# Optimization experiments

Measured on AMD Instinct MI355X. Metric: run time of the kernel, lower is better.

Reference implementation:

```python
import jax, jax.numpy as jnp
import numpy as np
jax.config.update("jax_enable_x64", True)

B, N, FEAT_DIM, OUT_DIM = 16, 10000, 256, 256
CH = [3, 64, 64, 64, 128, FEAT_DIM]  # ptlk PointNet_features MLP widths (scale=1)
BN_EPS = 1e-5
L2_EPS = 1e-12


def setup_inputs() -> dict:
    key = jax.random.key(0)
    ks = jax.random.split(key, 2 * len(CH) + 4)
    inp = {"points": jax.random.normal(ks[0], (B, N, 3), dtype=jnp.float32)}
    for i in range(5):
        cin, cout = CH[i], CH[i + 1]
        inp[f"W{i}"] = jax.random.normal(ks[1 + 2 * i], (cout, cin), dtype=jnp.float32) / np.sqrt(cin).astype(np.float32)
        inp[f"g{i}"] = jnp.ones((cout,), jnp.float32)
        inp[f"b{i}"] = jnp.zeros((cout,), jnp.float32)
    inp["Wfc"] = jax.random.normal(ks[-2], (OUT_DIM, FEAT_DIM * FEAT_DIM), dtype=jnp.float32) / np.sqrt(FEAT_DIM * FEAT_DIM).astype(np.float32)
    inp["bfc"] = jnp.zeros((OUT_DIM,), jnp.float32)
    return inp


def _bn_relu(y, g, b):
    # training-mode BatchNorm1d over (batch, points) per channel; y: [B,C,N]
    mu = jnp.mean(y, axis=(0, 2), keepdims=True)
    var = jnp.var(y, axis=(0, 2), keepdims=True)
    y = (y - mu) * jax.lax.rsqrt(var + BN_EPS)
    return jax.nn.relu(y * g[None, :, None] + b[None, :, None])


def reference(points, W0, g0, b0, W1, g1, b1, W2, g2, b2, W3, g3, b3, W4, g4, b4, Wfc, bfc):
    x = jnp.transpose(points, (0, 2, 1))  # [B,3,N]
    for W, g, b in ((W0, g0, b0), (W1, g1, b1), (W2, g2, b2), (W3, g3, b3), (W4, g4, b4)):
        x = jnp.einsum('oc,bcn->bon', W, x)  # 1x1 conv1d
        x = _bn_relu(x, g, b)
    f = jnp.transpose(x, (0, 2, 1))  # [B,N,D] per-point features
    # so_cov: global mean over all B*N points (as in the original), then per-batch covariance
    mean = jnp.mean(f.reshape(-1, FEAT_DIM), axis=0)  # [D]
    fc = f - mean
    cov = jnp.einsum('bnd,bne->bde', fc, fc) / np.float32(N)  # [B,D,D]
    # matrix square-root via fp64 SVD (torch: x.double(); u s v = svd; u diag(s^0.5) v^T)
    u, s, vh = jnp.linalg.svd(cov.astype(jnp.float64), full_matrices=False)
    sqrt_cov = (u * jnp.sqrt(s)[:, None, :]) @ vh  # [B,D,D]
    v = sqrt_cov.reshape(f.shape[0], FEAT_DIM * FEAT_DIM).astype(jnp.float32)
    out = v @ Wfc.T + bfc  # [B,OUT_DIM]
    norm = jnp.maximum(jnp.linalg.norm(out, axis=-1, keepdims=True), L2_EPS)
    return out / norm
```

## Files before the change

### kernel.cpp

```cpp
#include <hip/hip_runtime.h>
#include <cmath>

constexpr int NB   = 16;
constexpr int NPTS = 10000;
constexpr int NBN  = NB * NPTS;
constexpr int NS_ITERS = 18;
constexpr int COV_CHUNKS = 20;
constexpr int CHUNK_PTS  = 500;
constexpr int COV_KK     = 16;

typedef _Float16 f16x8 __attribute__((ext_vector_type(8)));
typedef float  f32x4  __attribute__((ext_vector_type(4)));
typedef unsigned short ushort4v __attribute__((ext_vector_type(4)));
typedef unsigned short ushort8v __attribute__((ext_vector_type(8)));

__global__ __launch_bounds__(256) void conv0_ker(const float* __restrict__ pts,
                                                 const float* __restrict__ W,
                                                 float* __restrict__ y) {
    int g = blockIdx.x * 256 + threadIdx.x;
    int b = g / NPTS;
    int n = g - b * NPTS;
    float p0 = pts[3 * (size_t)g + 0];
    float p1 = pts[3 * (size_t)g + 1];
    float p2 = pts[3 * (size_t)g + 2];
    float* yp = y + ((size_t)b * 64) * NPTS + n;
    for (int o = 0; o < 64; ++o) {
        float v = W[3 * o] * p0 + W[3 * o + 1] * p1 + W[3 * o + 2] * p2;
        yp[(size_t)o * NPTS] = v;
    }
}

__device__ __forceinline__ unsigned short f2h(float f) {
    return __builtin_bit_cast(unsigned short, (_Float16)f);
}
__device__ __forceinline__ float hres(float f) {
    return f - (float)(_Float16)f;
}
__device__ __forceinline__ int swzu(int us) {
    return us ^ (((us >> 7) & 3) << 4);
}

template <int CIN, int COUT, int OTILE>
__global__ __launch_bounds__(256) void conv_mfma(const float* __restrict__ xin,
                                                 const float* __restrict__ ss,
                                                 const float* __restrict__ W,
                                                 float* __restrict__ y) {
    constexpr int OT = OTILE / 16;
    constexpr int WM = 4;
    constexpr int WN = (OTILE == 128) ? 4 : 2;
    __shared__ unsigned short Xp[2][8 * 512];
    __shared__ unsigned short Wp[2][OT * 512];

    const int tid  = threadIdx.x;
    const int lane = tid & 63;
    const int w    = tid >> 6;
    const int wr   = (OTILE == 128) ? (w & 1) : 0;
    const int wc   = (OTILE == 128) ? (w >> 1) : w;

    const int nb = blockIdx.x * 128;
    const int ob = blockIdx.y * OTILE;
    const int b  = blockIdx.z;

    f32x4 acc[WM][WN];
#pragma unroll
    for (int m = 0; m < WM; ++m)
#pragma unroll
        for (int n = 0; n < WN; ++n) acc[m][n] = (f32x4){0.f, 0.f, 0.f, 0.f};

    const int xn = tid & 127;
    const int th = tid >> 7;
    const bool nok = (nb + xn) < NPTS;

#pragma unroll 1
    for (int kc = 0; kc < CIN; kc += 32) {
        __syncthreads();
#pragma unroll
        for (int i = 0; i < OTILE / 32; ++i) {
            int l = i * 256 + tid;
            int o = l >> 3, k4 = (l & 7) << 2;
            float4 v = *(const float4*)(W + (size_t)(ob + o) * CIN + kc + k4);
            ushort4v h4, l4;
            h4[0] = f2h(v.x); l4[0] = f2h(hres(v.x));
            h4[1] = f2h(v.y); l4[1] = f2h(hres(v.y));
            h4[2] = f2h(v.z); l4[2] = f2h(hres(v.z));
            h4[3] = f2h(v.w); l4[3] = f2h(hres(v.w));
            int us = swzu((o >> 4) * 512 + ((k4 >> 3) * 16 + (o & 15)) * 8 + (k4 & 7));
            *(ushort4v*)&Wp[0][us] = h4;
            *(ushort4v*)&Wp[1][us] = l4;
        }
#pragma unroll
        for (int qq = 0; qq < 2; ++qq) {
            int q = th * 2 + qq;
            const float* xb = xin + ((size_t)(b * CIN + kc + q * 8)) * NPTS + nb + xn;
            float f[8];
#pragma unroll
            for (int j = 0; j < 8; ++j) {
                float v = nok ? xb[(size_t)j * NPTS] : 0.f;
                int c = kc + q * 8 + j;
                f[j] = fmaxf(fmaf(v, ss[c], ss[256 + c]), 0.f);
            }
            ushort8v h8, l8;
#pragma unroll
            for (int j = 0; j < 8; ++j) {
                h8[j] = f2h(f[j]);
                l8[j] = f2h(hres(f[j]));
            }
            int us = swzu((xn >> 4) * 512 + (q * 16 + (xn & 15)) * 8);
            *(ushort8v*)&Xp[0][us] = h8;
            *(ushort8v*)&Xp[1][us] = l8;
        }
        __syncthreads();

        f16x8 ah[WM], al[WM], bh[WN], bl[WN];
#pragma unroll
        for (int m = 0; m < WM; ++m) {
            int us = swzu((wr * WM + m) * 512 + lane * 8);
            ah[m] = *(const f16x8*)&Wp[0][us];
            al[m] = *(const f16x8*)&Wp[1][us];
        }
#pragma unroll
        for (int n = 0; n < WN; ++n) {
            int us = swzu((wc * WN + n) * 512 + lane * 8);
            bh[n] = *(const f16x8*)&Xp[0][us];
            bl[n] = *(const f16x8*)&Xp[1][us];
        }
#pragma unroll
        for (int m = 0; m < WM; ++m)
#pragma unroll
            for (int n = 0; n < WN; ++n) {
                acc[m][n] = __builtin_amdgcn_mfma_f32_16x16x32_f16(ah[m], bh[n], acc[m][n], 0, 0, 0);
                acc[m][n] = __builtin_amdgcn_mfma_f32_16x16x32_f16(ah[m], bl[n], acc[m][n], 0, 0, 0);
                acc[m][n] = __builtin_amdgcn_mfma_f32_16x16x32_f16(al[m], bh[n], acc[m][n], 0, 0, 0);
            }
    }

    const int ro = (lane >> 4) * 4;
    const int co = lane & 15;
#pragma unroll
    for (int m = 0; m < WM; ++m) {
        int o = ob + wr * (WM * 16) + m * 16 + ro;
#pragma unroll
        for (int n = 0; n < WN; ++n) {
            int col = nb + wc * (WN * 16) + n * 16 + co;
            if (col < NPTS) {
                float* yp = y + ((size_t)(b * COUT + o)) * NPTS + col;
#pragma unroll
                for (int r = 0; r < 4; ++r)
                    yp[(size_t)r * NPTS] = acc[m][n][r];
            }
        }
    }
}

__global__ void chan_stats(const float* __restrict__ y, int C, float* __restrict__ stats) {
    int c = blockIdx.x, b = blockIdx.y, t = threadIdx.x;
    const float* p = y + ((size_t)(b * C + c)) * NPTS;
    float s = 0.f, q = 0.f;
    for (int n = t; n < NPTS; n += 256) {
        float v = p[n];
        s += v;
        q = fmaf(v, v, q);
    }
    for (int off = 32; off; off >>= 1) {
        s += __shfl_down(s, off);
        q += __shfl_down(q, off);
    }
    __shared__ float ls[4], lq[4];
    if ((t & 63) == 0) { ls[t >> 6] = s; lq[t >> 6] = q; }
    __syncthreads();
    if (t == 0) {
        atomicAdd(&stats[c],     ls[0] + ls[1] + ls[2] + ls[3]);
        atomicAdd(&stats[C + c], lq[0] + lq[1] + lq[2] + lq[3]);
    }
}

__global__ void bn_finalize(const float* __restrict__ stats, const float* __restrict__ g,
                            const float* __restrict__ bi, int C, float* __restrict__ ss) {
    int c = threadIdx.x;
    if (c < C) {
        float mu  = stats[c] * (1.f / NBN);
        float var = stats[C + c] * (1.f / NBN) - mu * mu;
        float r = rsqrtf(var + 1e-5f);
        float s = g[c] * r;
        ss[c] = s;
        ss[256 + c] = bi[c] - mu * s;
    }
}

__device__ __forceinline__ int swz8(int byteoff) {
    return byteoff ^ (((byteoff >> 8) & 3) << 5);
}

__global__ __launch_bounds__(256) void cov_mfma(const float* __restrict__ y4,
                                                const float* __restrict__ ss,
                                                float* __restrict__ covP,
                                                float* __restrict__ fsumb) {
    __shared__ unsigned short pan[2][2][4096];

    const int chunk = blockIdx.x;
    const int tile  = blockIdx.y;
    const int b     = blockIdx.z;
    const int ti = (tile == 1) ? 1 : 0;
    const int tj = (tile == 0) ? 0 : 1;
    const int npan = (tile == 2) ? 2 : 1;

    const int tid  = threadIdx.x;
    const int lane = tid & 63;
    const int w    = tid >> 6;
    const int wr   = w & 1, wc = w >> 1;

    const int n0c = chunk * CHUNK_PTS;

    f32x4 acc[4][4];
#pragma unroll
    for (int m = 0; m < 4; ++m)
#pragma unroll
        for (int n = 0; n < 4; ++n) acc[m][n] = (f32x4){0.f, 0.f, 0.f, 0.f};

    const int g   = tid & 7;
    const int chb = tid >> 3;
    const int p4  = g * 4;
    const int q   = p4 >> 3, j0 = p4 & 7;

    float fs[4] = {0.f, 0.f, 0.f, 0.f};

#pragma unroll 1
    for (int kk = 0; kk < COV_KK; ++kk) {
        const int nbase = n0c + kk * 32;
        __syncthreads();
        for (int p = 0; p < npan; ++p) {
            const int pcb = (p ? tj : ti) * 128;
#pragma unroll
            for (int i = 0; i < 4; ++i) {
                const int ch = chb + 32 * i;
                float4 v = make_float4(0.f, 0.f, 0.f, 0.f);
                if (kk * 32 + p4 < CHUNK_PTS) {
                    v = *(const float4*)(y4 + ((size_t)(b * 256 + pcb + ch)) * NPTS + nbase + p4);
                    float sc = ss[pcb + ch], sh = ss[256 + pcb + ch];
                    v.x = fmaxf(fmaf(v.x, sc, sh), 0.f);
                    v.y = fmaxf(fmaf(v.y, sc, sh), 0.f);
                    v.z = fmaxf(fmaf(v.z, sc, sh), 0.f);
                    v.w = fmaxf(fmaf(v.w, sc, sh), 0.f);
                }
                if (npan == 1) fs[i] += (v.x + v.y) + (v.z + v.w);
                ushort4v h4, l4;
                h4[0] = f2h(v.x); l4[0] = f2h(hres(v.x));
                h4[1] = f2h(v.y); l4[1] = f2h(hres(v.y));
                h4[2] = f2h(v.z); l4[2] = f2h(hres(v.z));
                h4[3] = f2h(v.w); l4[3] = f2h(hres(v.w));
                const int addr = (ch >> 4) * 512 + (q * 16 + (ch & 15)) * 8 + j0;
                const int sa = swz8(addr * 2) >> 1;
                *(ushort4v*)&pan[p][0][sa] = h4;
                *(ushort4v*)&pan[p][1][sa] = l4;
            }
        }
        __syncthreads();

        const unsigned short* Ah = pan[0][0];
        const unsigned short* Al = pan[0][1];
        const unsigned short* Bh = pan[npan - 1][0];
        const unsigned short* Bl = pan[npan - 1][1];

        f16x8 ah[4], al[4], bh[4], bl[4];
#pragma unroll
        for (int m = 0; m < 4; ++m) {
            int t8 = (wr * 4 + m) * 512 + lane * 8;
            int sa = swz8(t8 * 2) >> 1;
            ah[m] = *(const f16x8*)&Ah[sa];
            al[m] = *(const f16x8*)&Al[sa];
        }
#pragma unroll
        for (int n = 0; n < 4; ++n) {
            int t8 = (wc * 4 + n) * 512 + lane * 8;
            int sa = swz8(t8 * 2) >> 1;
            bh[n] = *(const f16x8*)&Bh[sa];
            bl[n] = *(const f16x8*)&Bl[sa];
        }
#pragma unroll
        for (int m = 0; m < 4; ++m)
#pragma unroll
            for (int n = 0; n < 4; ++n) {
                acc[m][n] = __builtin_amdgcn_mfma_f32_16x16x32_f16(ah[m], bh[n], acc[m][n], 0, 0, 0);
                acc[m][n] = __builtin_amdgcn_mfma_f32_16x16x32_f16(ah[m], bl[n], acc[m][n], 0, 0, 0);
                acc[m][n] = __builtin_amdgcn_mfma_f32_16x16x32_f16(al[m], bh[n], acc[m][n], 0, 0, 0);
            }
    }

    if (npan == 1) {
#pragma unroll
        for (int i = 0; i < 4; ++i) {
            float s = fs[i];
            s += __shfl_xor(s, 1);
            s += __shfl_xor(s, 2);
            s += __shfl_xor(s, 4);
            if (g == 0)
                atomicAdd(&fsumb[b * 256 + ti * 128 + chb + 32 * i], s);
        }
    }

    float* outp = covP + (((size_t)(chunk * NB + b) * 3 + tile) << 14);
    const int rowb = wr * 64;
    const int colb = wc * 64;
#pragma unroll
    for (int m = 0; m < 4; ++m)
#pragma unroll
        for (int n = 0; n < 4; ++n)
#pragma unroll
            for (int r = 0; r < 4; ++r) {
                int row = rowb + m * 16 + (lane >> 4) * 4 + r;
                int col = colb + n * 16 + (lane & 15);
                outp[(row << 7) + col] = acc[m][n][r];
            }
}

__global__ void covfin_ker(const float* __restrict__ covP, const float* __restrict__ fsumb,
                           float* __restrict__ Y0, float* __restrict__ trace) {
    int r = blockIdx.x, b = blockIdx.y, c = threadIdx.x;
    float fbr = fsumb[b * 256 + r] * (1.f / NPTS);
    float fbc = fsumb[b * 256 + c] * (1.f / NPTS);
    float mr = 0.f, mc = 0.f;
    for (int q = 0; q < NB; ++q) {
        mr += fsumb[q * 256 + r];
        mc += fsumb[q * 256 + c];
    }
    mr *= (1.f / NBN);
    mc *= (1.f / NBN);
    int tile, rr, cc;
    if (r < 128 && c < 128)        { tile = 0; rr = r;       cc = c; }
    else if (r >= 128 && c >= 128) { tile = 1; rr = r - 128; cc = c - 128; }
    else if (r < 128)              { tile = 2; rr = r;       cc = c - 128; }
    else                           { tile = 2; rr = c;       cc = r - 128; }
    size_t base = (((size_t)b * 3 + tile) << 14) + ((size_t)rr << 7) + cc;
    float m5 = 0.f;
#pragma unroll
    for (int q = 0; q < COV_CHUNKS; ++q)
        m5 += covP[(size_t)q * (NB * 3 * 16384) + base];
    float v = m5 * (1.f / NPTS) - fbr * mc - mr * fbc + mr * mc;
    Y0[((size_t)b << 16) + ((size_t)r << 8) + c] = v;
    if (c == r) atomicAdd(&trace[b], v);
}

__global__ void ns_init(float* __restrict__ Y0, float* __restrict__ Z0,
                        const float* __restrict__ trace) {
    int i = blockIdx.x * 256 + threadIdx.x;
    int b = i >> 16, rc = i & 65535;
    float inv = 1.f / trace[b];
    Y0[i] *= inv;
    Z0[i] = ((rc >> 8) == (rc & 255)) ? 1.f : 0.f;
}

__device__ __forceinline__ void ns_body(const float* __restrict__ Ab,
                                        const float* __restrict__ Bb,
                                        float* __restrict__ Ob,
                                        float scale, float diag, int tile, int tid,
                                        unsigned short* Ap0, unsigned short* Ap1,
                                        unsigned short* Bp0, unsigned short* Bp1) {
    const int lane = tid & 63;
    const int w    = tid >> 6;
    const int wr   = w & 1, wc = w >> 1;
    const int tr = (tile >> 2) * 64, tc = (tile & 3) * 64;

    f32x4 acc[2][2];
#pragma unroll
    for (int m = 0; m < 2; ++m)
#pragma unroll
        for (int n = 0; n < 2; ++n) acc[m][n] = (f32x4){0.f, 0.f, 0.f, 0.f};

    const int fA = tid & 63;
    const int kq = tid >> 6;

#pragma unroll 1
    for (int kc = 0; kc < 256; kc += 32) {
        __syncthreads();
        const float* ap = Ab + (size_t)(tr + fA) * 256 + kc + kq * 8;
        float av[8];
        *(float4*)&av[0] = *(const float4*)ap;
        *(float4*)&av[4] = *(const float4*)(ap + 4);
        const float* bp = Bb + (size_t)(kc + kq * 8) * 256 + tc + fA;
        float bv[8];
#pragma unroll
        for (int j = 0; j < 8; ++j) bv[j] = bp[(size_t)j * 256];
        ushort8v ah8, al8, bh8, bl8;
#pragma unroll
        for (int j = 0; j < 8; ++j) {
            ah8[j] = f2h(av[j]); al8[j] = f2h(hres(av[j]));
            bh8[j] = f2h(bv[j]); bl8[j] = f2h(hres(bv[j]));
        }
        const int ua = (fA >> 4) * 512 + (kq * 16 + (fA & 15)) * 8;
        *(ushort8v*)&Ap0[ua] = ah8;
        *(ushort8v*)&Ap1[ua] = al8;
        *(ushort8v*)&Bp0[ua] = bh8;
        *(ushort8v*)&Bp1[ua] = bl8;
        __syncthreads();

        f16x8 a_h[2], a_l[2], b_h[2], b_l[2];
#pragma unroll
        for (int m = 0; m < 2; ++m) {
            int u = (wr * 2 + m) * 512 + lane * 8;
            a_h[m] = *(const f16x8*)&Ap0[u];
            a_l[m] = *(const f16x8*)&Ap1[u];
        }
#pragma unroll
        for (int n = 0; n < 2; ++n) {
            int u = (wc * 2 + n) * 512 + lane * 8;
            b_h[n] = *(const f16x8*)&Bp0[u];
            b_l[n] = *(const f16x8*)&Bp1[u];
        }
#pragma unroll
        for (int m = 0; m < 2; ++m)
#pragma unroll
            for (int n = 0; n < 2; ++n) {
                acc[m][n] = __builtin_amdgcn_mfma_f32_16x16x32_f16(a_h[m], b_h[n], acc[m][n], 0, 0, 0);
                acc[m][n] = __builtin_amdgcn_mfma_f32_16x16x32_f16(a_h[m], b_l[n], acc[m][n], 0, 0, 0);
                acc[m][n] = __builtin_amdgcn_mfma_f32_16x16x32_f16(a_l[m], b_h[n], acc[m][n], 0, 0, 0);
            }
    }

    const int ro = (lane >> 4) * 4, co = lane & 15;
#pragma unroll
    for (int m = 0; m < 2; ++m)
#pragma unroll
        for (int n = 0; n < 2; ++n) {
            int row = tr + wr * 32 + m * 16 + ro;
            int col = tc + wc * 32 + n * 16 + co;
#pragma unroll
            for (int r = 0; r < 4; ++r) {
                float v = scale * acc[m][n][r] + (((row + r) == col) ? diag : 0.f);
                Ob[(size_t)(row + r) * 256 + col] = v;
            }
        }
}

__global__ __launch_bounds__(256) void ns_gemm(const float* __restrict__ A,
                                               const float* __restrict__ B,
                                               float* __restrict__ O,
                                               float scale, float diag) {
    __shared__ unsigned short Ap[2][2048], Bp[2][2048];
    size_t off = (size_t)blockIdx.y << 16;
    ns_body(A + off, B + off, O + off, scale, diag, blockIdx.x, threadIdx.x,
            Ap[0], Ap[1], Bp[0], Bp[1]);
}

__global__ __launch_bounds__(256) void ns_gemm_pair(const float* __restrict__ Y,
                                                    const float* __restrict__ Mm,
                                                    const float* __restrict__ Z,
                                                    float* __restrict__ Yn,
                                                    float* __restrict__ Zn) {
    __shared__ unsigned short Ap[2][2048], Bp[2][2048];
    size_t off = (size_t)blockIdx.y << 16;
    if (blockIdx.z == 0)
        ns_body(Y + off, Mm + off, Yn + off, 0.5f, 0.f, blockIdx.x, threadIdx.x,
                Ap[0], Ap[1], Bp[0], Bp[1]);
    else
        ns_body(Mm + off, Z + off, Zn + off, 0.5f, 0.f, blockIdx.x, threadIdx.x,
                Ap[0], Ap[1], Bp[0], Bp[1]);
}

__global__ __launch_bounds__(256) void fc_ker(const float* __restrict__ Yf,
                                              const float* __restrict__ trace,
                                              const float* __restrict__ Wfc,
                                              float* __restrict__ outpre) {
    int kc = blockIdx.x;
    int ot = blockIdx.y;
    int t = threadIdx.x;
    __shared__ float Wl[64][129];
    __shared__ float Vl[16][129];
#pragma unroll
    for (int i = 0; i < 32; ++i) {
        int l = i * 256 + t;
        int o = l >> 7, k = l & 127;
        Wl[o][k] = Wfc[(size_t)(ot * 64 + o) * 65536 + kc * 128 + k];
    }
#pragma unroll
    for (int i = 0; i < 8; ++i) {
        int l = i * 256 + t;
        int bb = l >> 7, k = l & 127;
        Vl[bb][k] = sqrtf(trace[bb]) * Yf[((size_t)bb << 16) + kc * 128 + k];
    }
    __syncthreads();
    int ol = t & 63, bg = t >> 6;
    float a0 = 0.f, a1 = 0.f, a2 = 0.f, a3 = 0.f;
    for (int k = 0; k < 128; ++k) {
        float w = Wl[ol][k];
        a0 = fmaf(w, Vl[bg * 4 + 0][k], a0);
        a1 = fmaf(w, Vl[bg * 4 + 1][k], a1);
        a2 = fmaf(w, Vl[bg * 4 + 2][k], a2);
        a3 = fmaf(w, Vl[bg * 4 + 3][k], a3);
    }
    int o = ot * 64 + ol;
    atomicAdd(&outpre[(bg * 4 + 0) * 256 + o], a0);
    atomicAdd(&outpre[(bg * 4 + 1) * 256 + o], a1);
    atomicAdd(&outpre[(bg * 4 + 2) * 256 + o], a2);
    atomicAdd(&outpre[(bg * 4 + 3) * 256 + o], a3);
}

__global__ void norm_ker(const float* __restrict__ outpre, const float* __restrict__ bfc,
                         float* __restrict__ dout) {
    int b = blockIdx.x, t = threadIdx.x;
    float v = outpre[b * 256 + t] + bfc[t];
    float q = v * v;
    for (int off = 32; off; off >>= 1) q += __shfl_xor(q, off);
    __shared__ float lq[4];
    __shared__ float snorm;
    if ((t & 63) == 0) lq[t >> 6] = q;
    __syncthreads();
    if (t == 0) snorm = fmaxf(sqrtf(lq[0] + lq[1] + lq[2] + lq[3]), 1e-12f);
    __syncthreads();
    dout[b * 256 + t] = v / snorm;
}

extern "C" void kernel_launch(void* const* d_in, const int* in_sizes, int n_in,
                              void* d_out, int out_size, void* d_ws, size_t ws_size,
                              hipStream_t stream) {
    (void)in_sizes; (void)n_in; (void)out_size; (void)ws_size;
    const float* pts = (const float*)d_in[0];
    const float* Wm[5]; const float* gm[5]; const float* bm[5];
    for (int i = 0; i < 5; ++i) {
        Wm[i] = (const float*)d_in[1 + 3 * i];
        gm[i] = (const float*)d_in[2 + 3 * i];
        bm[i] = (const float*)d_in[3 + 3 * i];
    }
    const float* Wfc = (const float*)d_in[16];
    const float* bfc = (const float*)d_in[17];

    float* ws     = (float*)d_ws;
    float* stats  = ws;
    float* fsumb  = ws + 2560;
    float* trace  = ws + 6656;
    float* outpre = ws + 6672;
    float* ss     = ws + 10768;
    float* R      = ws + 16384;
    float* P      = R;
    float* Q      = R + (size_t)NB * 256 * NPTS;
    float* covP   = Q;
    float* Y0     = R;
    float* Y1     = Y0 + 1048576;
    float* Z0     = Y1 + 1048576;
    float* Z1     = Z0 + 1048576;
    float* Mb     = Z1 + 1048576;

    hipMemsetAsync(ws, 0, 16384 * sizeof(float), stream);

    conv0_ker<<<dim3(NBN / 256), dim3(256), 0, stream>>>(pts, Wm[0], P);
    chan_stats<<<dim3(64, NB), dim3(256), 0, stream>>>(P, 64, stats);
    bn_finalize<<<dim3(1), dim3(256), 0, stream>>>(stats, gm[0], bm[0], 64, ss);
    conv_mfma<64, 64, 64><<<dim3(79, 1, NB), dim3(256), 0, stream>>>(P, ss, Wm[1], Q);
    chan_stats<<<dim3(64, NB), dim3(256), 0, stream>>>(Q, 64, stats + 512);
    bn_finalize<<<dim3(1), dim3(256), 0, stream>>>(stats + 512, gm[1], bm[1], 64, ss + 512);
    conv_mfma<64, 64, 64><<<dim3(79, 1, NB), dim3(256), 0, stream>>>(Q, ss + 512, Wm[2], P);
    chan_stats<<<dim3(64, NB), dim3(256), 0, stream>>>(P, 64, stats + 1024);
    bn_finalize<<<dim3(1), dim3(256), 0, stream>>>(stats + 1024, gm[2], bm[2], 64, ss + 1024);
    conv_mfma<64, 128, 128><<<dim3(79, 1, NB), dim3(256), 0, stream>>>(P, ss + 1024, Wm[3], Q);
    chan_stats<<<dim3(128, NB), dim3(256), 0, stream>>>(Q, 128, stats + 1536);
    bn_finalize<<<dim3(1), dim3(256), 0, stream>>>(stats + 1536, gm[3], bm[3], 128, ss + 1536);
    conv_mfma<128, 256, 128><<<dim3(79, 2, NB), dim3(256), 0, stream>>>(Q, ss + 1536, Wm[4], R);
    chan_stats<<<dim3(256, NB), dim3(256), 0, stream>>>(R, 256, stats + 2048);
    bn_finalize<<<dim3(1), dim3(256), 0, stream>>>(stats + 2048, gm[4], bm[4], 256, ss + 2048);

    cov_mfma<<<dim3(COV_CHUNKS, 3, NB), dim3(256), 0, stream>>>(R, ss + 2048, covP, fsumb);
    covfin_ker<<<dim3(256, NB), dim3(256), 0, stream>>>(covP, fsumb, Y0, trace);
    ns_init<<<dim3(4096), dim3(256), 0, stream>>>(Y0, Z0, trace);

    float* Yc = Y0; float* Zc = Z0; float* Yn = Y1; float* Zn = Z1;
    for (int it = 0; it < NS_ITERS; ++it) {
        ns_gemm<<<dim3(16, NB), dim3(256), 0, stream>>>(Zc, Yc, Mb, -1.f, 3.f);
        ns_gemm_pair<<<dim3(16, NB, 2), dim3(256), 0, stream>>>(Yc, Mb, Zc, Yn, Zn);
        float* ty = Yc; Yc = Yn; Yn = ty;
        float* tz = Zc; Zc = Zn; Zn = tz;
    }

    fc_ker<<<dim3(512, 4), dim3(256), 0, stream>>>(Yc, trace, Wfc, outpre);
    norm_ker<<<dim3(NB), dim3(256), 0, stream>>>(outpre, bfc, (float*)d_out);
}
```

Before: 1.007 ms.

## Fuse BN stats into conv epilogue and persist Newton-Schulz loop

Computes per-channel sum and sum-of-squares inside the conv_mfma epilogue through shuffle reductions, LDS staging and atomics, which removes the separate chan_stats passes over the large activation tensors. It also replaces the 36 Newton-Schulz GEMM launches plus the init kernel with one persistent kernel of 256 blocks that synchronises through a hand-written atomic grid barrier. The barrier relies on all 256 blocks being co-resident, and its counters sit in the memset workspace region. The final result pointer becomes Y0 because the iteration count is even. In the fused loop each block now runs the Y and Z updates one after the other, so the work per barrier phase is serialised.

```diff
diff --git a/kernel.cpp b/kernel.cpp
--- a/kernel.cpp
+++ b/kernel.cpp
@@ -8,6 +8,7 @@
 constexpr int COV_CHUNKS = 20;
 constexpr int CHUNK_PTS  = 500;
 constexpr int COV_KK     = 16;
+constexpr unsigned NS_BLOCKS = 256;
 
 typedef _Float16 f16x8 __attribute__((ext_vector_type(8)));
 typedef float  f32x4  __attribute__((ext_vector_type(4)));
@@ -44,10 +45,12 @@
 __global__ __launch_bounds__(256) void conv_mfma(const float* __restrict__ xin,
                                                  const float* __restrict__ ss,
                                                  const float* __restrict__ W,
-                                                 float* __restrict__ y) {
+                                                 float* __restrict__ y,
+                                                 float* __restrict__ stats) {
     constexpr int OT = OTILE / 16;
     constexpr int WM = 4;
     constexpr int WN = (OTILE == 128) ? 4 : 2;
+    constexpr int NCW = (OTILE == 128) ? 2 : 4;
     __shared__ unsigned short Xp[2][8 * 512];
     __shared__ unsigned short Wp[2][OT * 512];
 
@@ -149,6 +152,42 @@
                     yp[(size_t)r * NPTS] = acc[m][n][r];
             }
         }
+    }
+
+    __syncthreads();
+    float* sbuf = (float*)&Xp[0][0];
+    float* qbuf = sbuf + NCW * OTILE;
+#pragma unroll
+    for (int m = 0; m < WM; ++m)
+#pragma unroll
+        for (int r = 0; r < 4; ++r) {
+            float s = 0.f, q = 0.f;
+#pragma unroll
+            for (int n = 0; n < WN; ++n) {
+                int col = nb + wc * (WN * 16) + n * 16 + co;
+                float v = acc[m][n][r];
+                if (col < NPTS) { s += v; q = fmaf(v, v, q); }
+            }
+            s += __shfl_xor(s, 1); q += __shfl_xor(q, 1);
+            s += __shfl_xor(s, 2); q += __shfl_xor(q, 2);
+            s += __shfl_xor(s, 4); q += __shfl_xor(q, 4);
+            s += __shfl_xor(s, 8); q += __shfl_xor(q, 8);
+            if (co == 0) {
+                int rowl = wr * (WM * 16) + m * 16 + ro + r;
+                sbuf[wc * OTILE + rowl] = s;
+                qbuf[wc * OTILE + rowl] = q;
+            }
+        }
+    __syncthreads();
+    if (tid < OTILE) {
+        float s = 0.f, q = 0.f;
+#pragma unroll
+        for (int j = 0; j < NCW; ++j) {
+            s += sbuf[j * OTILE + tid];
+            q += qbuf[j * OTILE + tid];
+        }
+        atomicAdd(&stats[ob + tid], s);
+        atomicAdd(&stats[COUT + ob + tid], q);
     }
 }
 
@@ -340,15 +379,6 @@
     if (c == r) atomicAdd(&trace[b], v);
 }
 
-__global__ void ns_init(float* __restrict__ Y0, float* __restrict__ Z0,
-                        const float* __restrict__ trace) {
-    int i = blockIdx.x * 256 + threadIdx.x;
-    int b = i >> 16, rc = i & 65535;
-    float inv = 1.f / trace[b];
-    Y0[i] *= inv;
-    Z0[i] = ((rc >> 8) == (rc & 255)) ? 1.f : 0.f;
-}
-
 __device__ __forceinline__ void ns_body(const float* __restrict__ Ab,
                                         const float* __restrict__ Bb,
                                         float* __restrict__ Ob,
@@ -431,29 +461,60 @@
         }
 }
 
-__global__ __launch_bounds__(256) void ns_gemm(const float* __restrict__ A,
-                                               const float* __restrict__ B,
-                                               float* __restrict__ O,
-                                               float scale, float diag) {
+__device__ __forceinline__ void grid_bar(unsigned int* bar, unsigned int nb) {
+    __syncthreads();
+    if (threadIdx.x == 0) {
+        __threadfence();
+        __hip_atomic_fetch_add(bar, 1u, __ATOMIC_ACQ_REL, __HIP_MEMORY_SCOPE_AGENT);
+        while (__hip_atomic_load(bar, __ATOMIC_ACQUIRE, __HIP_MEMORY_SCOPE_AGENT) < nb) {
+            __builtin_amdgcn_s_sleep(8);
+        }
+        __threadfence();
+    }
+    __syncthreads();
+}
+
+__global__ __launch_bounds__(256) void ns_fused(float* __restrict__ Y0, float* __restrict__ Z0,
+                                                float* __restrict__ Y1, float* __restrict__ Z1,
+                                                float* __restrict__ Mb,
+                                                const float* __restrict__ trace,
+                                                unsigned int* __restrict__ bar) {
     __shared__ unsigned short Ap[2][2048], Bp[2][2048];
-    size_t off = (size_t)blockIdx.y << 16;
-    ns_body(A + off, B + off, O + off, scale, diag, blockIdx.x, threadIdx.x,
-            Ap[0], Ap[1], Bp[0], Bp[1]);
-}
-
-__global__ __launch_bounds__(256) void ns_gemm_pair(const float* __restrict__ Y,
-                                                    const float* __restrict__ Mm,
-                                                    const float* __restrict__ Z,
-                                                    float* __restrict__ Yn,
-                                                    float* __restrict__ Zn) {
-    __shared__ unsigned short Ap[2][2048], Bp[2][2048];
-    size_t off = (size_t)blockIdx.y << 16;
-    if (blockIdx.z == 0)
-        ns_body(Y + off, Mm + off, Yn + off, 0.5f, 0.f, blockIdx.x, threadIdx.x,
+
+    const int bid  = blockIdx.x;
+    const int b    = bid >> 4;
+    const int tile = bid & 15;
+    const int t    = threadIdx.x;
+    const size_t off = (size_t)b << 16;
+    int bi = 0;
+
+    {
+        float inv = 1.f / trace[b];
+        int tr = (tile >> 2) * 64, tc = (tile & 3) * 64;
+#pragma unroll
+        for (int i = 0; i < 16; ++i) {
+            int l = i * 256 + t;
+            int r = tr + (l >> 6), c = tc + (l & 63);
+            size_t idx = off + ((size_t)r << 8) + c;
+            Y0[idx] *= inv;
+            Z0[idx] = (r == c) ? 1.f : 0.f;
+        }
+    }
+    grid_bar(&bar[bi++], NS_BLOCKS);
+
+    float* Yc = Y0; float* Zc = Z0; float* Yn = Y1; float* Zn = Z1;
+    for (int it = 0; it < NS_ITERS; ++it) {
+        ns_body(Zc + off, Yc + off, Mb + off, -1.f, 3.f, tile, t,
                 Ap[0], Ap[1], Bp[0], Bp[1]);
-    else
-        ns_body(Mm + off, Z + off, Zn + off, 0.5f, 0.f, blockIdx.x, threadIdx.x,
+        grid_bar(&bar[bi++], NS_BLOCKS);
+        ns_body(Yc + off, Mb + off, Yn + off, 0.5f, 0.f, tile, t,
                 Ap[0], Ap[1], Bp[0], Bp[1]);
+        ns_body(Mb + off, Zc + off, Zn + off, 0.5f, 0.f, tile, t,
+                Ap[0], Ap[1], Bp[0], Bp[1]);
+        grid_bar(&bar[bi++], NS_BLOCKS);
+        float* ty = Yc; Yc = Yn; Yn = ty;
+        float* tz = Zc; Zc = Zn; Zn = tz;
+    }
 }
 
 __global__ __launch_bounds__(256) void fc_ker(const float* __restrict__ Yf,
@@ -529,6 +590,7 @@
     float* trace  = ws + 6656;
     float* outpre = ws + 6672;
     float* ss     = ws + 10768;
+    unsigned int* bar = (unsigned int*)(ws + 13400);
     float* R      = ws + 16384;
     float* P      = R;
     float* Q      = R + (size_t)NB * 256 * NPTS;
@@ -544,31 +606,20 @@
     conv0_ker<<<dim3(NBN / 256), dim3(256), 0, stream>>>(pts, Wm[0], P);
     chan_stats<<<dim3(64, NB), dim3(256), 0, stream>>>(P, 64, stats);
     bn_finalize<<<dim3(1), dim3(256), 0, stream>>>(stats, gm[0], bm[0], 64, ss);
-    conv_mfma<64, 64, 64><<<dim3(79, 1, NB), dim3(256), 0, stream>>>(P, ss, Wm[1], Q);
-    chan_stats<<<dim3(64, NB), dim3(256), 0, stream>>>(Q, 64, stats + 512);
+    conv_mfma<64, 64, 64><<<dim3(79, 1, NB), dim3(256), 0, stream>>>(P, ss, Wm[1], Q, stats + 512);
     bn_finalize<<<dim3(1), dim3(256), 0, stream>>>(stats + 512, gm[1], bm[1], 64, ss + 512);
-    conv_mfma<64, 64, 64><<<dim3(79, 1, NB), dim3(256), 0, stream>>>(Q, ss + 512, Wm[2], P);
-    chan_stats<<<dim3(64, NB), dim3(256), 0, stream>>>(P, 64, stats + 1024);
+    conv_mfma<64, 64, 64><<<dim3(79, 1, NB), dim3(256), 0, stream>>>(Q, ss + 512, Wm[2], P, stats + 1024);
     bn_finalize<<<dim3(1), dim3(256), 0, stream>>>(stats + 1024, gm[2], bm[2], 64, ss + 1024);
-    conv_mfma<64, 128, 128><<<dim3(79, 1, NB), dim3(256), 0, stream>>>(P, ss + 1024, Wm[3], Q);
-    chan_stats<<<dim3(128, NB), dim3(256), 0, stream>>>(Q, 128, stats + 1536);
+    conv_mfma<64, 128, 128><<<dim3(79, 1, NB), dim3(256), 0, stream>>>(P, ss + 1024, Wm[3], Q, stats + 1536);
     bn_finalize<<<dim3(1), dim3(256), 0, stream>>>(stats + 1536, gm[3], bm[3], 128, ss + 1536);
-    conv_mfma<128, 256, 128><<<dim3(79, 2, NB), dim3(256), 0, stream>>>(Q, ss + 1536, Wm[4], R);
-    chan_stats<<<dim3(256, NB), dim3(256), 0, stream>>>(R, 256, stats + 2048);
+    conv_mfma<128, 256, 128><<<dim3(79, 2, NB), dim3(256), 0, stream>>>(Q, ss + 1536, Wm[4], R, stats + 2048);
     bn_finalize<<<dim3(1), dim3(256), 0, stream>>>(stats + 2048, gm[4], bm[4], 256, ss + 2048);
 
     cov_mfma<<<dim3(COV_CHUNKS, 3, NB), dim3(256), 0, stream>>>(R, ss + 2048, covP, fsumb);
     covfin_ker<<<dim3(256, NB), dim3(256), 0, stream>>>(covP, fsumb, Y0, trace);
-    ns_init<<<dim3(4096), dim3(256), 0, stream>>>(Y0, Z0, trace);
-
-    float* Yc = Y0; float* Zc = Z0; float* Yn = Y1; float* Zn = Z1;
-    for (int it = 0; it < NS_ITERS; ++it) {
-        ns_gemm<<<dim3(16, NB), dim3(256), 0, stream>>>(Zc, Yc, Mb, -1.f, 3.f);
-        ns_gemm_pair<<<dim3(16, NB, 2), dim3(256), 0, stream>>>(Yc, Mb, Zc, Yn, Zn);
-        float* ty = Yc; Yc = Yn; Yn = ty;
-        float* tz = Zc; Zc = Zn; Zn = tz;
-    }
-
-    fc_ker<<<dim3(512, 4), dim3(256), 0, stream>>>(Yc, trace, Wfc, outpre);
+
+    ns_fused<<<dim3(NS_BLOCKS), dim3(256), 0, stream>>>(Y0, Z0, Y1, Z1, Mb, trace, bar);
+
+    fc_ker<<<dim3(512, 4), dim3(256), 0, stream>>>(Y0, trace, Wfc, outpre);
     norm_ker<<<dim3(NB), dim3(256), 0, stream>>>(outpre, bfc, (float*)d_out);
 }
```

Result: slower. 2.278 ms (+126.1%).

## Fuse BN channel stats into conv epilogue and restage Newton-Schulz GEMM loads

Applied to the files above, without the earlier changes.

The conv_mfma kernels now reduce per-channel sum and sum-of-squares from their accumulators in the epilogue and atomically add them into the stats buffer. This removes four separate chan_stats passes that re-read large activation tensors. Separately, the Newton-Schulz GEMM body now stages B in shared memory for 128-wide K halves and loads and splits A directly into registers, which cuts barriers and A staging. The costs are float atomics (non-deterministic summation order) and larger shared-memory use per block.

```diff
diff --git a/kernel.cpp b/kernel.cpp
--- a/kernel.cpp
+++ b/kernel.cpp
@@ -44,10 +44,12 @@
 __global__ __launch_bounds__(256) void conv_mfma(const float* __restrict__ xin,
                                                  const float* __restrict__ ss,
                                                  const float* __restrict__ W,
-                                                 float* __restrict__ y) {
+                                                 float* __restrict__ y,
+                                                 float* __restrict__ stats) {
     constexpr int OT = OTILE / 16;
     constexpr int WM = 4;
     constexpr int WN = (OTILE == 128) ? 4 : 2;
+    constexpr int NCW = (OTILE == 128) ? 2 : 4;
     __shared__ unsigned short Xp[2][8 * 512];
     __shared__ unsigned short Wp[2][OT * 512];
 
@@ -149,6 +151,42 @@
                     yp[(size_t)r * NPTS] = acc[m][n][r];
             }
         }
+    }
+
+    __syncthreads();
+    float* sbuf = (float*)&Xp[0][0];
+    float* qbuf = sbuf + NCW * OTILE;
+#pragma unroll
+    for (int m = 0; m < WM; ++m)
+#pragma unroll
+        for (int r = 0; r < 4; ++r) {
+            float s = 0.f, q = 0.f;
+#pragma unroll
+            for (int n = 0; n < WN; ++n) {
+                int col = nb + wc * (WN * 16) + n * 16 + co;
+                float v = acc[m][n][r];
+                if (col < NPTS) { s += v; q = fmaf(v, v, q); }
+            }
+            s += __shfl_xor(s, 1); q += __shfl_xor(q, 1);
+            s += __shfl_xor(s, 2); q += __shfl_xor(q, 2);
+            s += __shfl_xor(s, 4); q += __shfl_xor(q, 4);
+            s += __shfl_xor(s, 8); q += __shfl_xor(q, 8);
+            if (co == 0) {
+                int rowl = wr * (WM * 16) + m * 16 + ro + r;
+                sbuf[wc * OTILE + rowl] = s;
+                qbuf[wc * OTILE + rowl] = q;
+            }
+        }
+    __syncthreads();
+    if (tid < OTILE) {
+        float s = 0.f, q = 0.f;
+#pragma unroll
+        for (int j = 0; j < NCW; ++j) {
+            s += sbuf[j * OTILE + tid];
+            q += qbuf[j * OTILE + tid];
+        }
+        atomicAdd(&stats[ob + tid], s);
+        atomicAdd(&stats[COUT + ob + tid], q);
     }
 }
 
@@ -349,71 +387,83 @@
     Z0[i] = ((rc >> 8) == (rc & 255)) ? 1.f : 0.f;
 }
 
-__device__ __forceinline__ void ns_body(const float* __restrict__ Ab,
-                                        const float* __restrict__ Bb,
-                                        float* __restrict__ Ob,
-                                        float scale, float diag, int tile, int tid,
-                                        unsigned short* Ap0, unsigned short* Ap1,
-                                        unsigned short* Bp0, unsigned short* Bp1) {
+__device__ __forceinline__ void ns_body2(const float* __restrict__ Ab,
+                                         const float* __restrict__ Bb,
+                                         float* __restrict__ Ob,
+                                         float scale, float diag, int tile, int tid,
+                                         unsigned short* Bp0, unsigned short* Bp1) {
     const int lane = tid & 63;
     const int w    = tid >> 6;
     const int wr   = w & 1, wc = w >> 1;
     const int tr = (tile >> 2) * 64, tc = (tile & 3) * 64;
 
-    f32x4 acc[2][2];
-#pragma unroll
-    for (int m = 0; m < 2; ++m)
-#pragma unroll
-        for (int n = 0; n < 2; ++n) acc[m][n] = (f32x4){0.f, 0.f, 0.f, 0.f};
-
     const int fA = tid & 63;
     const int kq = tid >> 6;
 
+    f32x4 acc[2][2];
+#pragma unroll
+    for (int m = 0; m < 2; ++m)
+#pragma unroll
+        for (int n = 0; n < 2; ++n) acc[m][n] = (f32x4){0.f, 0.f, 0.f, 0.f};
+
 #pragma unroll 1
-    for (int kc = 0; kc < 256; kc += 32) {
+    for (int half = 0; half < 2; ++half) {
         __syncthreads();
-        const float* ap = Ab + (size_t)(tr + fA) * 256 + kc + kq * 8;
-        float av[8];
-        *(float4*)&av[0] = *(const float4*)ap;
-        *(float4*)&av[4] = *(const float4*)(ap + 4);
-        const float* bp = Bb + (size_t)(kc + kq * 8) * 256 + tc + fA;
-        float bv[8];
-#pragma unroll
-        for (int j = 0; j < 8; ++j) bv[j] = bp[(size_t)j * 256];
-        ushort8v ah8, al8, bh8, bl8;
-#pragma unroll
-        for (int j = 0; j < 8; ++j) {
-            ah8[j] = f2h(av[j]); al8[j] = f2h(hres(av[j]));
-            bh8[j] = f2h(bv[j]); bl8[j] = f2h(hres(bv[j]));
-        }
-        const int ua = (fA >> 4) * 512 + (kq * 16 + (fA & 15)) * 8;
-        *(ushort8v*)&Ap0[ua] = ah8;
-        *(ushort8v*)&Ap1[ua] = al8;
-        *(ushort8v*)&Bp0[ua] = bh8;
-        *(ushort8v*)&Bp1[ua] = bl8;
+#pragma unroll
+        for (int kb = 0; kb < 4; ++kb) {
+            const int k0 = half * 128 + kb * 32 + kq * 8;
+            const float* bp = Bb + (size_t)k0 * 256 + tc + fA;
+            float bv[8];
+#pragma unroll
+            for (int j = 0; j < 8; ++j) bv[j] = bp[(size_t)j * 256];
+            ushort8v bh8, bl8;
+#pragma unroll
+            for (int j = 0; j < 8; ++j) {
+                bh8[j] = f2h(bv[j]);
+                bl8[j] = f2h(hres(bv[j]));
+            }
+            const int ua = ((fA >> 4) * 4 + kb) * 512 + (kq * 16 + (fA & 15)) * 8;
+            *(ushort8v*)&Bp0[ua] = bh8;
+            *(ushort8v*)&Bp1[ua] = bl8;
+        }
         __syncthreads();
 
-        f16x8 a_h[2], a_l[2], b_h[2], b_l[2];
-#pragma unroll
-        for (int m = 0; m < 2; ++m) {
-            int u = (wr * 2 + m) * 512 + lane * 8;
-            a_h[m] = *(const f16x8*)&Ap0[u];
-            a_l[m] = *(const f16x8*)&Ap1[u];
-        }
-#pragma unroll
-        for (int n = 0; n < 2; ++n) {
-            int u = (wc * 2 + n) * 512 + lane * 8;
-            b_h[n] = *(const f16x8*)&Bp0[u];
-            b_l[n] = *(const f16x8*)&Bp1[u];
-        }
-#pragma unroll
-        for (int m = 0; m < 2; ++m)
+#pragma unroll
+        for (int kk = 0; kk < 4; ++kk) {
+            f16x8 a_h[2], a_l[2];
+#pragma unroll
+            for (int m = 0; m < 2; ++m) {
+                const float* ap = Ab
+                    + (size_t)(tr + (wr * 2 + m) * 16 + (lane & 15)) * 256
+                    + half * 128 + kk * 32 + (lane >> 4) * 8;
+                float av[8];
+                *(float4*)&av[0] = *(const float4*)ap;
+                *(float4*)&av[4] = *(const float4*)(ap + 4);
+                ushort8v h8, l8;
+#pragma unroll
+                for (int j = 0; j < 8; ++j) {
+                    h8[j] = f2h(av[j]);
+                    l8[j] = f2h(hres(av[j]));
+                }
+                a_h[m] = __builtin_bit_cast(f16x8, h8);
+                a_l[m] = __builtin_bit_cast(f16x8, l8);
+            }
+            f16x8 b_h[2], b_l[2];
 #pragma unroll
             for (int n = 0; n < 2; ++n) {
-                acc[m][n] = __builtin_amdgcn_mfma_f32_16x16x32_f16(a_h[m], b_h[n], acc[m][n], 0, 0, 0);
-                acc[m][n] = __builtin_amdgcn_mfma_f32_16x16x32_f16(a_h[m], b_l[n], acc[m][n], 0, 0, 0);
-                acc[m][n] = __builtin_amdgcn_mfma_f32_16x16x32_f16(a_l[m], b_h[n], acc[m][n], 0, 0, 0);
-            }
+                int u = ((wc * 2 + n) * 4 + kk) * 512 + lane * 8;
+                b_h[n] = *(const f16x8*)&Bp0[u];
+                b_l[n] = *(const f16x8*)&Bp1[u];
+            }
+#pragma unroll
+            for (int m = 0; m < 2; ++m)
+#pragma unroll
+                for (int n = 0; n < 2; ++n) {
+                    acc[m][n] = __builtin_amdgcn_mfma_f32_16x16x32_f16(a_h[m], b_h[n], acc[m][n], 0, 0, 0);
+                    acc[m][n] = __builtin_amdgcn_mfma_f32_16x16x32_f16(a_h[m], b_l[n], acc[m][n], 0, 0, 0);
+                    acc[m][n] = __builtin_amdgcn_mfma_f32_16x16x32_f16(a_l[m], b_h[n], acc[m][n], 0, 0, 0);
+                }
+        }
     }
 
     const int ro = (lane >> 4) * 4, co = lane & 15;
@@ -435,10 +485,10 @@
                                                const float* __restrict__ B,
                                                float* __restrict__ O,
                                                float scale, float diag) {
-    __shared__ unsigned short Ap[2][2048], Bp[2][2048];
+    __shared__ unsigned short Bp[2][8192];
     size_t off = (size_t)blockIdx.y << 16;
-    ns_body(A + off, B + off, O + off, scale, diag, blockIdx.x, threadIdx.x,
-            Ap[0], Ap[1], Bp[0], Bp[1]);
+    ns_body2(A + off, B + off, O + off, scale, diag, blockIdx.x, threadIdx.x,
+             Bp[0], Bp[1]);
 }
 
 __global__ __launch_bounds__(256) void ns_gemm_pair(const float* __restrict__ Y,
@@ -446,14 +496,14 @@
                                                     const float* __restrict__ Z,
                                                     float* __restrict__ Yn,
                                                     float* __restrict__ Zn) {
-    __shared__ unsigned short Ap[2][2048], Bp[2][2048];
+    __shared__ unsigned short Bp[2][8192];
     size_t off = (size_t)blockIdx.y << 16;
     if (blockIdx.z == 0)
-        ns_body(Y + off, Mm + off, Yn + off, 0.5f, 0.f, blockIdx.x, threadIdx.x,
-                Ap[0], Ap[1], Bp[0], Bp[1]);
+        ns_body2(Y + off, Mm + off, Yn + off, 0.5f, 0.f, blockIdx.x, threadIdx.x,
+                 Bp[0], Bp[1]);
     else
-        ns_body(Mm + off, Z + off, Zn + off, 0.5f, 0.f, blockIdx.x, threadIdx.x,
-                Ap[0], Ap[1], Bp[0], Bp[1]);
+        ns_body2(Mm + off, Z + off, Zn + off, 0.5f, 0.f, blockIdx.x, threadIdx.x,
+                 Bp[0], Bp[1]);
 }
 
 __global__ __launch_bounds__(256) void fc_ker(const float* __restrict__ Yf,
@@ -544,17 +594,13 @@
     conv0_ker<<<dim3(NBN / 256), dim3(256), 0, stream>>>(pts, Wm[0], P);
     chan_stats<<<dim3(64, NB), dim3(256), 0, stream>>>(P, 64, stats);
     bn_finalize<<<dim3(1), dim3(256), 0, stream>>>(stats, gm[0], bm[0], 64, ss);
-    conv_mfma<64, 64, 64><<<dim3(79, 1, NB), dim3(256), 0, stream>>>(P, ss, Wm[1], Q);
-    chan_stats<<<dim3(64, NB), dim3(256), 0, stream>>>(Q, 64, stats + 512);
+    conv_mfma<64, 64, 64><<<dim3(79, 1, NB), dim3(256), 0, stream>>>(P, ss, Wm[1], Q, stats + 512);
     bn_finalize<<<dim3(1), dim3(256), 0, stream>>>(stats + 512, gm[1], bm[1], 64, ss + 512);
-    conv_mfma<64, 64, 64><<<dim3(79, 1, NB), dim3(256), 0, stream>>>(Q, ss + 512, Wm[2], P);
-    chan_stats<<<dim3(64, NB), dim3(256), 0, stream>>>(P, 64, stats + 1024);
+    conv_mfma<64, 64, 64><<<dim3(79, 1, NB), dim3(256), 0, stream>>>(Q, ss + 512, Wm[2], P, stats + 1024);
     bn_finalize<<<dim3(1), dim3(256), 0, stream>>>(stats + 1024, gm[2], bm[2], 64, ss + 1024);
-    conv_mfma<64, 128, 128><<<dim3(79, 1, NB), dim3(256), 0, stream>>>(P, ss + 1024, Wm[3], Q);
-    chan_stats<<<dim3(128, NB), dim3(256), 0, stream>>>(Q, 128, stats + 1536);
+    conv_mfma<64, 128, 128><<<dim3(79, 1, NB), dim3(256), 0, stream>>>(P, ss + 1024, Wm[3], Q, stats + 1536);
     bn_finalize<<<dim3(1), dim3(256), 0, stream>>>(stats + 1536, gm[3], bm[3], 128, ss + 1536);
-    conv_mfma<128, 256, 128><<<dim3(79, 2, NB), dim3(256), 0, stream>>>(Q, ss + 1536, Wm[4], R);
-    chan_stats<<<dim3(256, NB), dim3(256), 0, stream>>>(R, 256, stats + 2048);
+    conv_mfma<128, 256, 128><<<dim3(79, 2, NB), dim3(256), 0, stream>>>(Q, ss + 1536, Wm[4], R, stats + 2048);
     bn_finalize<<<dim3(1), dim3(256), 0, stream>>>(stats + 2048, gm[4], bm[4], 256, ss + 2048);
 
     cov_mfma<<<dim3(COV_CHUNKS, 3, NB), dim3(256), 0, stream>>>(R, ss + 2048, covP, fsumb);
```

Result: slower. 1.109 ms (+10.1%).

## Fuse BN channel stats into conv epilogue and prefetch cov loads

Applied to the files above, without the earlier changes.

Each conv_mfma block now reduces per-channel sum and sum-of-squares from its accumulators, combines them through LDS and adds them atomically. This removes the separate chan_stats passes that reread every activation tensor. The cov kernel is templated on panel count, split into two launches, and software-pipelined: the next chunk's global loads are issued before the MFMA phase, with raw barriers replacing __syncthreads. The cost is more atomics, more register pressure from the prefetch buffers, and float summation order that differs from before.

```diff
diff --git a/kernel.cpp b/kernel.cpp
--- a/kernel.cpp
+++ b/kernel.cpp
@@ -39,15 +39,20 @@
 __device__ __forceinline__ int swzu(int us) {
     return us ^ (((us >> 7) & 3) << 4);
 }
+__device__ __forceinline__ int swz8(int byteoff) {
+    return byteoff ^ (((byteoff >> 8) & 3) << 5);
+}
 
 template <int CIN, int COUT, int OTILE>
 __global__ __launch_bounds__(256) void conv_mfma(const float* __restrict__ xin,
                                                  const float* __restrict__ ss,
                                                  const float* __restrict__ W,
-                                                 float* __restrict__ y) {
+                                                 float* __restrict__ y,
+                                                 float* __restrict__ stats) {
     constexpr int OT = OTILE / 16;
     constexpr int WM = 4;
     constexpr int WN = (OTILE == 128) ? 4 : 2;
+    constexpr int NCW = (OTILE == 128) ? 2 : 4;
     __shared__ unsigned short Xp[2][8 * 512];
     __shared__ unsigned short Wp[2][OT * 512];
 
@@ -150,6 +155,42 @@
             }
         }
     }
+
+    __syncthreads();
+    float* sbuf = (float*)&Xp[0][0];
+    float* qbuf = sbuf + NCW * OTILE;
+#pragma unroll
+    for (int m = 0; m < WM; ++m)
+#pragma unroll
+        for (int r = 0; r < 4; ++r) {
+            float s = 0.f, q = 0.f;
+#pragma unroll
+            for (int n = 0; n < WN; ++n) {
+                int col = nb + wc * (WN * 16) + n * 16 + co;
+                float v = acc[m][n][r];
+                if (col < NPTS) { s += v; q = fmaf(v, v, q); }
+            }
+            s += __shfl_xor(s, 1); q += __shfl_xor(q, 1);
+            s += __shfl_xor(s, 2); q += __shfl_xor(q, 2);
+            s += __shfl_xor(s, 4); q += __shfl_xor(q, 4);
+            s += __shfl_xor(s, 8); q += __shfl_xor(q, 8);
+            if (co == 0) {
+                int rowl = wr * (WM * 16) + m * 16 + ro + r;
+                sbuf[wc * OTILE + rowl] = s;
+                qbuf[wc * OTILE + rowl] = q;
+            }
+        }
+    __syncthreads();
+    if (tid < OTILE) {
+        float s = 0.f, q = 0.f;
+#pragma unroll
+        for (int j = 0; j < NCW; ++j) {
+            s += sbuf[j * OTILE + tid];
+            q += qbuf[j * OTILE + tid];
+        }
+        atomicAdd(&stats[ob + tid], s);
+        atomicAdd(&stats[COUT + ob + tid], q);
+    }
 }
 
 __global__ void chan_stats(const float* __restrict__ y, int C, float* __restrict__ stats) {
@@ -187,29 +228,43 @@
     }
 }
 
-__device__ __forceinline__ int swz8(int byteoff) {
-    return byteoff ^ (((byteoff >> 8) & 3) << 5);
-}
-
+template <int NPAN>
+__device__ __forceinline__ void cov_issue(const float* __restrict__ y4, int b,
+                                          int ti, int tj, int chb, int p4,
+                                          int n0c, int kk, float4 (&cur)[NPAN][4]) {
+    const int nbase = n0c + kk * 32;
+#pragma unroll
+    for (int p = 0; p < NPAN; ++p) {
+        const int pcb = (p ? tj : ti) * 128;
+#pragma unroll
+        for (int i = 0; i < 4; ++i) {
+            const int ch = chb + 32 * i;
+            float4 v = make_float4(0.f, 0.f, 0.f, 0.f);
+            if (kk * 32 + p4 < CHUNK_PTS)
+                v = *(const float4*)(y4 + ((size_t)(b * 256 + pcb + ch)) * NPTS + nbase + p4);
+            cur[p][i] = v;
+        }
+    }
+}
+
+template <int NPAN>
 __global__ __launch_bounds__(256) void cov_mfma(const float* __restrict__ y4,
                                                 const float* __restrict__ ss,
                                                 float* __restrict__ covP,
                                                 float* __restrict__ fsumb) {
-    __shared__ unsigned short pan[2][2][4096];
+    __shared__ unsigned short pan[NPAN][2][4096];
 
     const int chunk = blockIdx.x;
-    const int tile  = blockIdx.y;
+    const int tile  = (NPAN == 2) ? 2 : (int)blockIdx.y;
     const int b     = blockIdx.z;
     const int ti = (tile == 1) ? 1 : 0;
     const int tj = (tile == 0) ? 0 : 1;
-    const int npan = (tile == 2) ? 2 : 1;
 
     const int tid  = threadIdx.x;
     const int lane = tid & 63;
     const int w    = tid >> 6;
     const int wr   = w & 1, wc = w >> 1;
-
-    const int n0c = chunk * CHUNK_PTS;
+    const int n0c  = chunk * CHUNK_PTS;
 
     f32x4 acc[4][4];
 #pragma unroll
@@ -223,26 +278,34 @@
     const int q   = p4 >> 3, j0 = p4 & 7;
 
     float fs[4] = {0.f, 0.f, 0.f, 0.f};
+    float4 cur[NPAN][4];
+
+    cov_issue<NPAN>(y4, b, ti, tj, chb, p4, n0c, 0, cur);
 
 #pragma unroll 1
     for (int kk = 0; kk < COV_KK; ++kk) {
-        const int nbase = n0c + kk * 32;
-        __syncthreads();
-        for (int p = 0; p < npan; ++p) {
+        __builtin_amdgcn_sched_barrier(0);
+        __builtin_amdgcn_s_barrier();
+        __builtin_amdgcn_sched_barrier(0);
+
+        const bool ok = (kk * 32 + p4 < CHUNK_PTS);
+#pragma unroll
+        for (int p = 0; p < NPAN; ++p) {
             const int pcb = (p ? tj : ti) * 128;
 #pragma unroll
             for (int i = 0; i < 4; ++i) {
                 const int ch = chb + 32 * i;
-                float4 v = make_float4(0.f, 0.f, 0.f, 0.f);
-                if (kk * 32 + p4 < CHUNK_PTS) {
-                    v = *(const float4*)(y4 + ((size_t)(b * 256 + pcb + ch)) * NPTS + nbase + p4);
+                float4 v = cur[p][i];
+                if (ok) {
                     float sc = ss[pcb + ch], sh = ss[256 + pcb + ch];
                     v.x = fmaxf(fmaf(v.x, sc, sh), 0.f);
                     v.y = fmaxf(fmaf(v.y, sc, sh), 0.f);
                     v.z = fmaxf(fmaf(v.z, sc, sh), 0.f);
                     v.w = fmaxf(fmaf(v.w, sc, sh), 0.f);
+                } else {
+                    v = make_float4(0.f, 0.f, 0.f, 0.f);
                 }
-                if (npan == 1) fs[i] += (v.x + v.y) + (v.z + v.w);
+                if (NPAN == 1) fs[i] += (v.x + v.y) + (v.z + v.w);
                 ushort4v h4, l4;
                 h4[0] = f2h(v.x); l4[0] = f2h(hres(v.x));
                 h4[1] = f2h(v.y); l4[1] = f2h(hres(v.y));
@@ -254,12 +317,17 @@
                 *(ushort4v*)&pan[p][1][sa] = l4;
             }
         }
-        __syncthreads();
+        if (kk + 1 < COV_KK)
+            cov_issue<NPAN>(y4, b, ti, tj, chb, p4, n0c, kk + 1, cur);
+
+        asm volatile("s_waitcnt lgkmcnt(0)" ::: "memory");
+        __builtin_amdgcn_s_barrier();
+        __builtin_amdgcn_sched_barrier(0);
 
         const unsigned short* Ah = pan[0][0];
         const unsigned short* Al = pan[0][1];
-        const unsigned short* Bh = pan[npan - 1][0];
-        const unsigned short* Bl = pan[npan - 1][1];
+        const unsigned short* Bh = pan[NPAN - 1][0];
+        const unsigned short* Bl = pan[NPAN - 1][1];
 
         f16x8 ah[4], al[4], bh[4], bl[4];
 #pragma unroll
@@ -286,7 +354,7 @@
             }
     }
 
-    if (npan == 1) {
+    if (NPAN == 1) {
 #pragma unroll
         for (int i = 0; i < 4; ++i) {
             float s = fs[i];
@@ -544,20 +612,17 @@
     conv0_ker<<<dim3(NBN / 256), dim3(256), 0, stream>>>(pts, Wm[0], P);
     chan_stats<<<dim3(64, NB), dim3(256), 0, stream>>>(P, 64, stats);
     bn_finalize<<<dim3(1), dim3(256), 0, stream>>>(stats, gm[0], bm[0], 64, ss);
-    conv_mfma<64, 64, 64><<<dim3(79, 1, NB), dim3(256), 0, stream>>>(P, ss, Wm[1], Q);
-    chan_stats<<<dim3(64, NB), dim3(256), 0, stream>>>(Q, 64, stats + 512);
+    conv_mfma<64, 64, 64><<<dim3(79, 1, NB), dim3(256), 0, stream>>>(P, ss, Wm[1], Q, stats + 512);
     bn_finalize<<<dim3(1), dim3(256), 0, stream>>>(stats + 512, gm[1], bm[1], 64, ss + 512);
-    conv_mfma<64, 64, 64><<<dim3(79, 1, NB), dim3(256), 0, stream>>>(Q, ss + 512, Wm[2], P);
-    chan_stats<<<dim3(64, NB), dim3(256), 0, stream>>>(P, 64, stats + 1024);
+    conv_mfma<64, 64, 64><<<dim3(79, 1, NB), dim3(256), 0, stream>>>(Q, ss + 512, Wm[2], P, stats + 1024);
     bn_finalize<<<dim3(1), dim3(256), 0, stream>>>(stats + 1024, gm[2], bm[2], 64, ss + 1024);
-    conv_mfma<64, 128, 128><<<dim3(79, 1, NB), dim3(256), 0, stream>>>(P, ss + 1024, Wm[3], Q);
-    chan_stats<<<dim3(128, NB), dim3(256), 0, stream>>>(Q, 128, stats + 1536);
+    conv_mfma<64, 128, 128><<<dim3(79, 1, NB), dim3(256), 0, stream>>>(P, ss + 1024, Wm[3], Q, stats + 1536);
     bn_finalize<<<dim3(1), dim3(256), 0, stream>>>(stats + 1536, gm[3], bm[3], 128, ss + 1536);
-    conv_mfma<128, 256, 128><<<dim3(79, 2, NB), dim3(256), 0, stream>>>(Q, ss + 1536, Wm[4], R);
-    chan_stats<<<dim3(256, NB), dim3(256), 0, stream>>>(R, 256, stats + 2048);
+    conv_mfma<128, 256, 128><<<dim3(79, 2, NB), dim3(256), 0, stream>>>(Q, ss + 1536, Wm[4], R, stats + 2048);
     bn_finalize<<<dim3(1), dim3(256), 0, stream>>>(stats + 2048, gm[4], bm[4], 256, ss + 2048);
 
-    cov_mfma<<<dim3(COV_CHUNKS, 3, NB), dim3(256), 0, stream>>>(R, ss + 2048, covP, fsumb);
+    cov_mfma<1><<<dim3(COV_CHUNKS, 2, NB), dim3(256), 0, stream>>>(R, ss + 2048, covP, fsumb);
+    cov_mfma<2><<<dim3(COV_CHUNKS, 1, NB), dim3(256), 0, stream>>>(R, ss + 2048, covP, fsumb);
     covfin_ker<<<dim3(256, NB), dim3(256), 0, stream>>>(covP, fsumb, Y0, trace);
     ns_init<<<dim3(4096), dim3(256), 0, stream>>>(Y0, Z0, trace);
 
```

Result: no change. 1.014 ms (+0.7%).
